# Optimization experiments

Measured on AMD Instinct MI355X. Metric: run time of the kernel, lower is better.

Reference implementation:

```python
import jax, jax.numpy as jnp
import numpy as np

N = 50000   # nodes
E = 800000  # edges
F = 128     # feat_dim
I = 128     # internal_dim
G = 64      # graphs in batch
EPS = 1e-5


def setup_inputs() -> dict:
    key = jax.random.key(0)
    ks = jax.random.split(key, 32)
    s = 0.1
    inp = {
        'x': jax.random.normal(ks[0], (N, F), dtype=jnp.float32),
        'edge_index': jax.random.randint(ks[1], (2, E), 0, N, dtype=jnp.int64),
        'batch': jnp.sort(jax.random.randint(ks[2], (N,), 0, G, dtype=jnp.int64)),
        # InitialSubnet: Linear(F->I) + BN(I)
        'init_W': jax.random.normal(ks[3], (F, I)) * s,
        'init_b': jnp.zeros((I,)),
        'init_g': jnp.ones((I,)),
        'init_bt': jnp.zeros((I,)),
        # 2 middle EdgeConv subnets: Linear(2I->I) + BN(I)
        'mid_W': jax.random.normal(ks[4], (2, 2 * I, I)) * s,
        'mid_b': jnp.zeros((2, I)),
        'mid_g': jnp.ones((2, I)),
        'mid_bt': jnp.zeros((2, I)),
        # 1 er / 1 pr receptor-specific EdgeConv subnet each
        'er_W': jax.random.normal(ks[5], (1, 2 * I, I)) * s,
        'er_b': jnp.zeros((1, I)),
        'er_g': jnp.ones((1, I)),
        'er_bt': jnp.zeros((1, I)),
        'pr_W': jax.random.normal(ks[6], (1, 2 * I, I)) * s,
        'pr_b': jnp.zeros((1, I)),
        'pr_g': jnp.ones((1, I)),
        'pr_bt': jnp.zeros((1, I)),
        # 3 shared posts: Linear(I->2) + BN(2)
        'spost_W': jax.random.normal(ks[7], (3, I, 2)) * s,
        'spost_b': jnp.zeros((3, 2)),
        'spost_g': jnp.ones((3, 2)),
        'spost_bt': jnp.zeros((3, 2)),
        # 1 er post / 1 pr post: Linear(I->1) + BN(1)
        'erpost_W': jax.random.normal(ks[8], (1, I, 1)) * s,
        'erpost_b': jnp.zeros((1, 1)),
        'erpost_g': jnp.ones((1, 1)),
        'erpost_bt': jnp.zeros((1, 1)),
        'prpost_W': jax.random.normal(ks[9], (1, I, 1)) * s,
        'prpost_b': jnp.zeros((1, 1)),
        'prpost_g': jnp.ones((1, 1)),
        'prpost_bt': jnp.zeros((1, 1)),
    }
    return inp


def _bn(h, g, b):
    # BatchNorm1d in training mode: batch stats over the row dim, biased var
    m = jnp.mean(h, axis=0)
    v = jnp.var(h, axis=0)
    return (h - m) * jax.lax.rsqrt(v + EPS) * g + b


def _edgeconv(h, src, dst, W, b, g, bt):
    # PyG EdgeConv: msg = nn(cat([x_i, x_j - x_i])), aggr=max over incoming edges
    x_i = h[dst]                      # [E, I]
    x_j = h[src]                      # [E, I]
    msg = jnp.concatenate([x_i, x_j - x_i], axis=-1) @ W + b  # [E, I]
    msg = jax.nn.elu(_bn(msg, g, bt))
    out = jax.ops.segment_max(msg, dst, num_segments=N)
    return jnp.where(jnp.isneginf(out), 0.0, out)  # isolated nodes -> 0


def _post(h, batch, counts, W, b, g, bt):
    # elu(BN(Linear(h))) then global_mean_pool; dropout is identity (eval)
    h2 = jax.nn.elu(_bn(h @ W + b, g, bt))
    pooled = jax.ops.segment_sum(h2, batch, num_segments=G)
    return pooled / counts[:, None]


def reference(x, edge_index, batch,
              init_W, init_b, init_g, init_bt,
              mid_W, mid_b, mid_g, mid_bt,
              er_W, er_b, er_g, er_bt,
              pr_W, pr_b, pr_g, pr_bt,
              spost_W, spost_b, spost_g, spost_bt,
              erpost_W, erpost_b, erpost_g, erpost_bt,
              prpost_W, prpost_b, prpost_g, prpost_bt):
    src, dst = edge_index[0], edge_index[1]
    counts = jnp.maximum(jax.ops.segment_sum(jnp.ones((N,), x.dtype), batch, num_segments=G), 1.0)

    outs = []
    # InitialSubnet: gelu(BN(Linear(x)))
    h = jax.nn.gelu(_bn(x @ init_W + init_b, init_g, init_bt), approximate=False)
    outs.append(_post(h, batch, counts, spost_W[0], spost_b[0], spost_g[0], spost_bt[0]))

    for l in range(2):
        h = _edgeconv(h, src, dst, mid_W[l], mid_b[l], mid_g[l], mid_bt[l])
        outs.append(_post(h, batch, counts, spost_W[l + 1], spost_b[l + 1], spost_g[l + 1], spost_bt[l + 1]))

    er_h = h
    pr_h = h
    for l in range(1):
        er_h = _edgeconv(er_h, src, dst, er_W[l], er_b[l], er_g[l], er_bt[l])
        er_out = _post(er_h, batch, counts, erpost_W[l], erpost_b[l], erpost_g[l], erpost_bt[l])
        pr_h = _edgeconv(pr_h, src, dst, pr_W[l], pr_b[l], pr_g[l], pr_bt[l])
        pr_out = _post(pr_h, batch, counts, prpost_W[l], prpost_b[l], prpost_g[l], prpost_bt[l])
        outs.append(jnp.concatenate([er_out, pr_out], axis=-1))

    agg = outs[0]
    for o in outs[1:]:
        agg = agg + o
    return agg  # [G, 2]
```

## Files before the change

### kernel.cpp

```cpp
#include <hip/hip_runtime.h>
#include <math.h>

#define EPS 1e-5f

typedef float f32x4v __attribute__((ext_vector_type(4)));
typedef short s16x8  __attribute__((ext_vector_type(8)));

__device__ __forceinline__ float elu_f(float x) { return x > 0.f ? x : expm1f(x); }
__device__ __forceinline__ float blo(unsigned u) { return __uint_as_float(u << 16); }
__device__ __forceinline__ float bhi(unsigned u) { return __uint_as_float(u & 0xffff0000u); }
__device__ __forceinline__ unsigned f2b(float f) {
  unsigned u = __float_as_uint(f);
  unsigned r = ((u >> 16) & 1u) + 0x7fffu;
  return (u + r) >> 16;
}
__device__ __forceinline__ unsigned pack2(float a, float b) {
  return f2b(a) | (f2b(b) << 16);
}

__global__ __launch_bounds__(256) void prep_csr0(const float* __restrict__ init_W,
    const float* __restrict__ mid_W, const float* __restrict__ er_W,
    const float* __restrict__ pr_W, const float* __restrict__ mid_g,
    const float* __restrict__ er_g, const float* __restrict__ pr_g,
    unsigned short* __restrict__ WT,
    const int* __restrict__ dst, int* __restrict__ partials, int Ecnt,
    const int* __restrict__ batch, float* __restrict__ counts, int Nn) {
  if (blockIdx.x < 320) {
    int grp = blockIdx.x >> 6;
    int i = (blockIdx.x & 63) * 256 + threadIdx.x;
    if (i >= 16384) return;
    int k = i >> 7, c = i & 127;
    if (grp == 0) {
      WT[c * 128 + k] = (unsigned short)f2b(init_W[k * 128 + c]);
      return;
    }
    const float* W; const float* g; unsigned short* Wd; unsigned short* W2;
    if (grp == 1)      { W = mid_W;             g = mid_g;       Wd = WT + 1 * 16384; W2 = WT + 2 * 16384; }
    else if (grp == 2) { W = mid_W + 256 * 128; g = mid_g + 128; Wd = WT + 3 * 16384; W2 = WT + 4 * 16384; }
    else if (grp == 3) { W = er_W;              g = er_g;        Wd = WT + 5 * 16384; W2 = WT + 6 * 16384; }
    else               { W = pr_W;              g = pr_g;        Wd = WT + 7 * 16384; W2 = WT + 8 * 16384; }
    float sg = (g[c] >= 0.f) ? 1.f : -1.f;
    float w1 = W[k * 128 + c];
    float w2 = W[(k + 128) * 128 + c];
    Wd[c * 128 + k] = (unsigned short)f2b((w1 - w2) * sg);
    W2[c * 128 + k] = (unsigned short)f2b(w2 * sg);
  } else {
    int b = blockIdx.x - 320;
    if (b < 64) {
      __shared__ int cnt[256];
      cnt[threadIdx.x] = 0;
      __syncthreads();
      int i0 = b * 256 + threadIdx.x, stride = 64 * 256;
      for (int e = i0; e < Ecnt; e += stride) atomicAdd(&cnt[(unsigned)dst[e] >> 8], 1);
      __syncthreads();
      partials[b * 256 + threadIdx.x] = cnt[threadIdx.x];
    } else {
      __shared__ float lc[64];
      if (threadIdx.x < 64) lc[threadIdx.x] = 0.f;
      __syncthreads();
      int i0 = (b - 64) * 256 + threadIdx.x, stride = 64 * 256;
      for (int n = i0; n < Nn; n += stride) atomicAdd(&lc[batch[n]], 1.f);
      __syncthreads();
      if (threadIdx.x < 64 && lc[threadIdx.x] != 0.f)
        atomicAdd(&counts[threadIdx.x * 16], lc[threadIdx.x]);
    }
  }
}

__global__ __launch_bounds__(256) void csr_p0_scan(const int* __restrict__ partials,
    int nblk, int* __restrict__ bucket_base, int* __restrict__ gcursor) {
  __shared__ int sc[256];
  int b = threadIdx.x;
  int s = 0;
  for (int k = 0; k < nblk; ++k) s += partials[k * 256 + b];
  sc[b] = s;
  __syncthreads();
  for (int off = 1; off < 256; off <<= 1) {
    int t = (b >= off) ? sc[b - off] : 0;
    __syncthreads();
    sc[b] += t;
    __syncthreads();
  }
  int excl = sc[b] - s;
  bucket_base[b] = excl;
  gcursor[b * 16] = excl;
  if (b == 255) bucket_base[256] = sc[255];
}

#define P1_CHUNK 4096
__global__ __launch_bounds__(256) void csr_p1_bin(const int* __restrict__ src,
    const int* __restrict__ dst, int* __restrict__ gcursor,
    unsigned* __restrict__ binned, int Ecnt) {
  __shared__ unsigned stage[P1_CHUNK];
  __shared__ int cnt[256], lbase[256], gbase[256], lcur[256], sc[256];
  int tid = threadIdx.x;
  int e0 = blockIdx.x * P1_CHUNK;
  int ecnt = Ecnt - e0; if (ecnt > P1_CHUNK) ecnt = P1_CHUNK;
  cnt[tid] = 0;
  __syncthreads();
  for (int i = tid; i < ecnt; i += 256) atomicAdd(&cnt[(unsigned)dst[e0 + i] >> 8], 1);
  __syncthreads();
  sc[tid] = cnt[tid];
  __syncthreads();
  for (int off = 1; off < 256; off <<= 1) {
    int t = (tid >= off) ? sc[tid - off] : 0;
    __syncthreads();
    sc[tid] += t;
    __syncthreads();
  }
  lbase[tid] = sc[tid] - cnt[tid];
  lcur[tid] = lbase[tid];
  gbase[tid] = (cnt[tid] > 0) ? atomicAdd(&gcursor[tid * 16], cnt[tid]) : 0;
  __syncthreads();
  for (int i = tid; i < ecnt; i += 256) {
    int d = dst[e0 + i], s = src[e0 + i];
    int bk = (unsigned)d >> 8;
    int p = atomicAdd(&lcur[bk], 1);
    stage[p] = ((unsigned)bk << 24) | ((unsigned)(d & 255) << 16) | (unsigned)s;
  }
  __syncthreads();
  for (int i = tid; i < ecnt; i += 256) {
    unsigned v = stage[i];
    int bk = v >> 24;
    binned[gbase[bk] + (i - lbase[bk])] = v;
  }
}

#define P2_CAP 12288
__global__ __launch_bounds__(256) void csr_p2_sort(const unsigned* __restrict__ binned,
    const int* __restrict__ bucket_base, unsigned short* __restrict__ csr_src,
    int* __restrict__ deg, int* __restrict__ rowstart, int Nn) {
  __shared__ unsigned short stage[P2_CAP];
  __shared__ int cnt[256], lbase[256], lcur[256], sc[256];
  int b = blockIdx.x, tid = threadIdx.x;
  int base = bucket_base[b];
  int bcnt = bucket_base[b + 1] - base;
  if (bcnt > P2_CAP) bcnt = P2_CAP;
  cnt[tid] = 0;
  __syncthreads();
  for (int i = tid; i < bcnt; i += 256) atomicAdd(&cnt[(binned[base + i] >> 16) & 255], 1);
  __syncthreads();
  sc[tid] = cnt[tid];
  __syncthreads();
  for (int off = 1; off < 256; off <<= 1) {
    int t = (tid >= off) ? sc[tid - off] : 0;
    __syncthreads();
    sc[tid] += t;
    __syncthreads();
  }
  lbase[tid] = sc[tid] - cnt[tid];
  lcur[tid] = lbase[tid];
  int node = b * 256 + tid;
  if (node < Nn) { deg[node] = cnt[tid]; rowstart[node] = base + lbase[tid]; }
  __syncthreads();
  for (int i = tid; i < bcnt; i += 256) {
    unsigned v = binned[base + i];
    int j = (v >> 16) & 255;
    int p = atomicAdd(&lcur[j], 1);
    stage[p] = (unsigned short)(v & 0xffffu);
  }
  __syncthreads();
  for (int i = tid; i < bcnt; i += 256) csr_src[base + i] = stage[i];
}

template<int XF32, int NMAT, int STATS>
__global__ __launch_bounds__(256, 3) void gemm_mfma(const void* __restrict__ Xv,
    const unsigned short* __restrict__ W0t, const unsigned short* __restrict__ W1t,
    const unsigned short* __restrict__ W2t, const unsigned short* __restrict__ W3t,
    unsigned short* __restrict__ Y0, unsigned short* __restrict__ Y1,
    unsigned short* __restrict__ Y2, unsigned short* __restrict__ Y3,
    float* __restrict__ stOut, int Nrows) {
  int tid = threadIdx.x, lane = tid & 63, wv = tid >> 6;
  int r0 = blockIdx.x * 64;
  int rlo = lane & 15, kg = lane >> 4;
  s16x8 zf = {0, 0, 0, 0, 0, 0, 0, 0};
  s16x8 af[4][4];
#pragma unroll
  for (int rg = 0; rg < 4; ++rg) {
    int arow = r0 + rg * 16 + rlo;
    if (arow < Nrows) {
      if (XF32) {
        const float* xr = (const float*)Xv + (size_t)arow * 128 + kg * 8;
#pragma unroll
        for (int s2 = 0; s2 < 4; ++s2) {
          float4 a = *(const float4*)(xr + s2 * 32);
          float4 b = *(const float4*)(xr + s2 * 32 + 4);
          s16x8 t;
          t[0] = (short)f2b(a.x); t[1] = (short)f2b(a.y);
          t[2] = (short)f2b(a.z); t[3] = (short)f2b(a.w);
          t[4] = (short)f2b(b.x); t[5] = (short)f2b(b.y);
          t[6] = (short)f2b(b.z); t[7] = (short)f2b(b.w);
          af[rg][s2] = t;
        }
      } else {
        const unsigned short* xr = (const unsigned short*)Xv + (size_t)arow * 128 + kg * 8;
#pragma unroll
        for (int s2 = 0; s2 < 4; ++s2) af[rg][s2] = *(const s16x8*)(xr + s2 * 32);
      }
    } else {
#pragma unroll
      for (int s2 = 0; s2 < 4; ++s2) af[rg][s2] = zf;
    }
  }
  const unsigned short* Ws[4] = {W0t, W1t, W2t, W3t};
  unsigned short* Ys[4] = {Y0, Y1, Y2, Y3};
#pragma unroll
  for (int o = 0; o < NMAT; ++o) {
    const unsigned short* Wt = Ws[o];
    unsigned short* Y = Ys[o];
#pragma unroll
    for (int t = 0; t < 2; ++t) {
      int nt = wv * 2 + t;
      const unsigned short* wp = Wt + (size_t)(nt * 16 + rlo) * 128 + kg * 8;
      s16x8 wf[4];
#pragma unroll
      for (int s2 = 0; s2 < 4; ++s2) wf[s2] = *(const s16x8*)(wp + s2 * 32);
      f32x4v acc[4];
#pragma unroll
      for (int rg = 0; rg < 4; ++rg) acc[rg] = (f32x4v){0.f, 0.f, 0.f, 0.f};
#pragma unroll
      for (int s2 = 0; s2 < 4; ++s2)
#pragma unroll
        for (int rg = 0; rg < 4; ++rg)
          acc[rg] = __builtin_amdgcn_mfma_f32_16x16x32_bf16(wf[s2], af[rg][s2], acc[rg], 0, 0, 0);
      float ps0 = 0.f, ps1 = 0.f, ps2 = 0.f, ps3 = 0.f;
      float pq0 = 0.f, pq1 = 0.f, pq2 = 0.f, pq3 = 0.f;
#pragma unroll
      for (int rg = 0; rg < 4; ++rg) {
        int arow = r0 + rg * 16 + rlo;
        if (arow < Nrows) {
          uint2 ov;
          ov.x = pack2(acc[rg][0], acc[rg][1]);
          ov.y = pack2(acc[rg][2], acc[rg][3]);
          *(uint2*)(Y + (size_t)arow * 128 + nt * 16 + kg * 4) = ov;
          if (STATS) {
            float y0 = blo(ov.x), y1 = bhi(ov.x), y2 = blo(ov.y), y3 = bhi(ov.y);
            ps0 += y0; pq0 += y0 * y0;
            ps1 += y1; pq1 += y1 * y1;
            ps2 += y2; pq2 += y2 * y2;
            ps3 += y3; pq3 += y3 * y3;
          }
        }
      }
      if (STATS) {
#pragma unroll
        for (int off = 1; off < 16; off <<= 1) {
          ps0 += __shfl_xor(ps0, off); pq0 += __shfl_xor(pq0, off);
          ps1 += __shfl_xor(ps1, off); pq1 += __shfl_xor(pq1, off);
          ps2 += __shfl_xor(ps2, off); pq2 += __shfl_xor(pq2, off);
          ps3 += __shfl_xor(ps3, off); pq3 += __shfl_xor(pq3, off);
        }
        if (rlo == 0) {
          int col = nt * 16 + kg * 4;
          float* sb = stOut + (size_t)(blockIdx.x & 15) * 256;
          atomicAdd(&sb[2 * col + 0], ps0); atomicAdd(&sb[2 * col + 1], pq0);
          atomicAdd(&sb[2 * (col + 1)], ps1); atomicAdd(&sb[2 * (col + 1) + 1], pq1);
          atomicAdd(&sb[2 * (col + 2)], ps2); atomicAdd(&sb[2 * (col + 2) + 1], pq2);
          atomicAdd(&sb[2 * (col + 3)], ps3); atomicAdd(&sb[2 * (col + 3) + 1], pq3);
        }
      }
    }
  }
}

template<int NMAT, int ACT>
__global__ __launch_bounds__(256, 3) void gemm_act(const unsigned short* __restrict__ Xv,
    const unsigned short* __restrict__ W0t, const unsigned short* __restrict__ W1t,
    const unsigned short* __restrict__ W2t, const unsigned short* __restrict__ W3t,
    unsigned short* __restrict__ Y0, unsigned short* __restrict__ Y1,
    unsigned short* __restrict__ Y2, unsigned short* __restrict__ Y3,
    const float* __restrict__ stn, const float* __restrict__ g,
    const float* __restrict__ bt, const int* __restrict__ deg,
    const float* __restrict__ Wp, float* __restrict__ zP, float* __restrict__ stp,
    float invCnt, int Nrows) {
  __shared__ unsigned short hl[64][136];
  __shared__ float lsc[128], lsh[128], lw0[128], lw1[128];
  __shared__ float red[4][4];
  int tid = threadIdx.x, lane = tid & 63, wv = tid >> 6;
  int r0 = blockIdx.x * 64;
  int rlo = lane & 15, kg = lane >> 4;
  if (tid < 128) {
    float sm = 0.f, sq = 0.f;
#pragma unroll
    for (int k = 0; k < 16; ++k) {
      sm += stn[k * 256 + 2 * tid];
      sq += stn[k * 256 + 2 * tid + 1];
    }
    float mean = sm * invCnt;
    float var = sq * invCnt - mean * mean;
    float sc = g[tid] * rsqrtf(var + EPS);
    float sh = bt[tid] - mean * sc;
    if (ACT == 2 && g[tid] < 0.f) sc = -sc;
    lsc[tid] = sc; lsh[tid] = sh;
    lw0[tid] = Wp[tid * 2]; lw1[tid] = Wp[tid * 2 + 1];
  }
  __syncthreads();
  {
    int row = tid >> 2, q = tid & 3;
    int arow = r0 + row;
    bool rok = arow < Nrows;
    int lrow = rok ? arow : 0;
    float live = 1.f;
    if (ACT == 2) live = (rok && deg[arow] > 0) ? 1.f : 0.f;
    else live = rok ? 1.f : 0.f;
    const uint4* xr = (const uint4*)(Xv + (size_t)lrow * 128 + q * 32);
    float dd0 = 0.f, dd1 = 0.f;
#pragma unroll
    for (int b = 0; b < 4; ++b) {
      uint4 v = xr[b];
      unsigned w[4] = {v.x, v.y, v.z, v.w};
      int cb = q * 32 + b * 8;
#pragma unroll
      for (int u = 0; u < 4; ++u) {
        int c = cb + 2 * u;
        float t0 = blo(w[u]) * lsc[c] + lsh[c];
        float t1 = bhi(w[u]) * lsc[c + 1] + lsh[c + 1];
        float y0, y1;
        if (ACT == 1) {
          y0 = 0.5f * t0 * (1.f + erff(t0 * 0.70710678118f));
          y1 = 0.5f * t1 * (1.f + erff(t1 * 0.70710678118f));
        } else {
          y0 = elu_f(t0); y1 = elu_f(t1);
        }
        y0 *= live; y1 *= live;
        *(unsigned*)&hl[row][c] = pack2(y0, y1);
        dd0 += y0 * lw0[c] + y1 * lw0[c + 1];
        dd1 += y0 * lw1[c] + y1 * lw1[c + 1];
      }
    }
    dd0 += __shfl_xor(dd0, 1); dd0 += __shfl_xor(dd0, 2);
    dd1 += __shfl_xor(dd1, 1); dd1 += __shfl_xor(dd1, 2);
    if (q == 0 && rok) {
      zP[(size_t)arow * 2] = dd0;
      zP[(size_t)arow * 2 + 1] = dd1;
    }
    float s0v = (q == 0 && rok) ? dd0 : 0.f;
    float s1v = (q == 0 && rok) ? dd1 : 0.f;
    float q0v = s0v * s0v, q1v = s1v * s1v;
#pragma unroll
    for (int off = 4; off < 64; off <<= 1) {
      s0v += __shfl_xor(s0v, off); s1v += __shfl_xor(s1v, off);
      q0v += __shfl_xor(q0v, off); q1v += __shfl_xor(q1v, off);
    }
    if (lane == 0) { red[wv][0] = s0v; red[wv][1] = s1v; red[wv][2] = q0v; red[wv][3] = q1v; }
  }
  __syncthreads();
  if (tid < 4) {
    float v = red[0][tid] + red[1][tid] + red[2][tid] + red[3][tid];
    atomicAdd(&stp[tid * 64], v);
  }
  s16x8 af[4][4];
#pragma unroll
  for (int rg = 0; rg < 4; ++rg)
#pragma unroll
    for (int s2 = 0; s2 < 4; ++s2)
      af[rg][s2] = *(const s16x8*)&hl[rg * 16 + rlo][kg * 8 + s2 * 32];
  const unsigned short* Ws[4] = {W0t, W1t, W2t, W3t};
  unsigned short* Ys[4] = {Y0, Y1, Y2, Y3};
#pragma unroll
  for (int o = 0; o < NMAT; ++o) {
    const unsigned short* Wt = Ws[o];
    unsigned short* Y = Ys[o];
#pragma unroll
    for (int t = 0; t < 2; ++t) {
      int nt = wv * 2 + t;
      const unsigned short* wp = Wt + (size_t)(nt * 16 + rlo) * 128 + kg * 8;
      s16x8 wf[4];
#pragma unroll
      for (int s2 = 0; s2 < 4; ++s2) wf[s2] = *(const s16x8*)(wp + s2 * 32);
      f32x4v acc[4];
#pragma unroll
      for (int rg = 0; rg < 4; ++rg) acc[rg] = (f32x4v){0.f, 0.f, 0.f, 0.f};
#pragma unroll
      for (int s2 = 0; s2 < 4; ++s2)
#pragma unroll
        for (int rg = 0; rg < 4; ++rg)
          acc[rg] = __builtin_amdgcn_mfma_f32_16x16x32_bf16(wf[s2], af[rg][s2], acc[rg], 0, 0, 0);
#pragma unroll
      for (int rg = 0; rg < 4; ++rg) {
        int arow = r0 + rg * 16 + rlo;
        if (arow < Nrows) {
          uint2 ov;
          ov.x = pack2(acc[rg][0], acc[rg][1]);
          ov.y = pack2(acc[rg][2], acc[rg][3]);
          *(uint2*)(Y + (size_t)arow * 128 + nt * 16 + kg * 4) = ov;
        }
      }
    }
  }
}

__global__ __launch_bounds__(256, 8) void conv_pass(const unsigned short* __restrict__ A,
    const unsigned short* __restrict__ B, const unsigned short* __restrict__ csr_src,
    const int* __restrict__ rowstart, const int* __restrict__ deg,
    const float* __restrict__ g, unsigned short* __restrict__ Mx,
    float* __restrict__ st, int Nn, int convBlks,
    const float* __restrict__ zPp, const int* __restrict__ batch,
    const float* __restrict__ counts, const float* __restrict__ stpp,
    const float* __restrict__ g2, const float* __restrict__ bt2,
    float* __restrict__ out, float invN) {
  __shared__ float s_sum[128], s_ssq[128];
  int tid = threadIdx.x;
  if ((int)blockIdx.x >= convBlks) {
    __shared__ float lacc[128];
    if (tid < 128) lacc[tid] = 0.f;
    __syncthreads();
    float m0 = stpp[0] * invN, v0 = stpp[128] * invN - m0 * m0;
    float scale0 = g2[0] * rsqrtf(v0 + EPS), shift0 = bt2[0] - m0 * scale0;
    float m1 = stpp[64] * invN, v1 = stpp[192] * invN - m1 * m1;
    float scale1 = g2[1] * rsqrtf(v1 + EPS), shift1 = bt2[1] - m1 * scale1;
    int i0 = (blockIdx.x - convBlks) * 256 + tid;
    int stride = 32 * 256;
    for (int n = i0; n < Nn; n += stride) {
      int gi = batch[n];
      atomicAdd(&lacc[gi * 2], elu_f(zPp[n * 2] * scale0 + shift0));
      atomicAdd(&lacc[gi * 2 + 1], elu_f(zPp[n * 2 + 1] * scale1 + shift1));
    }
    __syncthreads();
    if (tid < 128) {
      int gi = tid >> 1, p = tid & 1;
      float v = lacc[tid];
      if (v != 0.f) atomicAdd(&out[gi * 2 + p], v / fmaxf(counts[gi * 16], 1.f));
    }
    return;
  }
  if (tid < 128) { s_sum[tid] = 0.f; s_ssq[tid] = 0.f; }
  __syncthreads();
  int lane = tid & 63;
  int wave = __builtin_amdgcn_readfirstlane((blockIdx.x << 2) + (tid >> 6));
  int wstride = convBlks << 2;
  int c0 = lane * 2;
  float sg0 = (g[c0] >= 0.f) ? 1.f : -1.f;
  float sg1 = (g[c0 + 1] >= 0.f) ? 1.f : -1.f;
  const unsigned* A32 = (const unsigned*)A;
  const unsigned* B32 = (const unsigned*)B;
  unsigned* M32 = (unsigned*)Mx;
  float s0 = 0.f, ss0 = 0.f, s1 = 0.f, ss1 = 0.f;
  for (int n = wave; n < Nn; n += wstride) {
    int dg = deg[n];
    if (dg == 0) continue;
    int beg = rowstart[n];
    unsigned ua = A32[(size_t)n * 64 + lane];
    float a0 = blo(ua), a1 = bhi(ua);
    float mx0 = -INFINITY, mx1 = -INFINITY;
    int e = beg, eend = beg + dg;
    for (; e + 8 <= eend; e += 8) {
      int idx[8];
#pragma unroll
      for (int q = 0; q < 8; ++q) idx[q] = csr_src[e + q];
      unsigned uu[8];
#pragma unroll
      for (int q = 0; q < 8; ++q) uu[q] = B32[(size_t)idx[q] * 64 + lane];
#pragma unroll
      for (int q = 0; q < 8; ++q) {
        float m0 = a0 + blo(uu[q]), m1 = a1 + bhi(uu[q]);
        s0 += m0; ss0 += m0 * m0;
        s1 += m1; ss1 += m1 * m1;
        mx0 = fmaxf(mx0, m0);
        mx1 = fmaxf(mx1, m1);
      }
    }
    for (; e + 2 <= eend; e += 2) {
      int ia = csr_src[e], ib = csr_src[e + 1];
      unsigned u0 = B32[(size_t)ia * 64 + lane];
      unsigned u1 = B32[(size_t)ib * 64 + lane];
      float m00 = a0 + blo(u0), m01 = a1 + bhi(u0);
      float m10 = a0 + blo(u1), m11 = a1 + bhi(u1);
      s0 += m00 + m10; ss0 += m00 * m00 + m10 * m10;
      s1 += m01 + m11; ss1 += m01 * m01 + m11 * m11;
      mx0 = fmaxf(mx0, fmaxf(m00, m10));
      mx1 = fmaxf(mx1, fmaxf(m01, m11));
    }
    if (e < eend) {
      unsigned u0 = B32[(size_t)csr_src[e] * 64 + lane];
      float m00 = a0 + blo(u0), m01 = a1 + bhi(u0);
      s0 += m00; ss0 += m00 * m00;
      s1 += m01; ss1 += m01 * m01;
      mx0 = fmaxf(mx0, m00);
      mx1 = fmaxf(mx1, m01);
    }
    M32[(size_t)n * 64 + lane] = pack2(mx0, mx1);
  }
  atomicAdd(&s_sum[c0], s0 * sg0); atomicAdd(&s_ssq[c0], ss0);
  atomicAdd(&s_sum[c0 + 1], s1 * sg1); atomicAdd(&s_ssq[c0 + 1], ss1);
  __syncthreads();
  if (tid < 128) {
    float* sb = st + (size_t)(blockIdx.x & 15) * 256;
    atomicAdd(&sb[2 * tid], s_sum[tid]);
    atomicAdd(&sb[2 * tid + 1], s_ssq[tid]);
  }
}

__global__ __launch_bounds__(256, 8) void conv_pass_dual(
    const unsigned short* __restrict__ Aer, const unsigned short* __restrict__ Ber,
    const unsigned short* __restrict__ Apr, const unsigned short* __restrict__ Bpr,
    const unsigned short* __restrict__ csr_src,
    const int* __restrict__ rowstart, const int* __restrict__ deg,
    const float* __restrict__ g_er, const float* __restrict__ g_pr,
    unsigned short* __restrict__ Mer, unsigned short* __restrict__ Mpr,
    float* __restrict__ st_er, float* __restrict__ st_pr, int Nn, int convBlks,
    const float* __restrict__ zPp, const int* __restrict__ batch,
    const float* __restrict__ counts, const float* __restrict__ stpp,
    const float* __restrict__ g2, const float* __restrict__ bt2,
    float* __restrict__ out, float invN) {
  __shared__ float s_e[256], s_p[256];
  int tid = threadIdx.x;
  if ((int)blockIdx.x >= convBlks) {
    __shared__ float lacc[128];
    if (tid < 128) lacc[tid] = 0.f;
    __syncthreads();
    float m0 = stpp[0] * invN, v0 = stpp[128] * invN - m0 * m0;
    float scale0 = g2[0] * rsqrtf(v0 + EPS), shift0 = bt2[0] - m0 * scale0;
    float m1 = stpp[64] * invN, v1 = stpp[192] * invN - m1 * m1;
    float scale1 = g2[1] * rsqrtf(v1 + EPS), shift1 = bt2[1] - m1 * scale1;
    int i0 = (blockIdx.x - convBlks) * 256 + tid;
    int stride = 32 * 256;
    for (int n = i0; n < Nn; n += stride) {
      int gi = batch[n];
      atomicAdd(&lacc[gi * 2], elu_f(zPp[n * 2] * scale0 + shift0));
      atomicAdd(&lacc[gi * 2 + 1], elu_f(zPp[n * 2 + 1] * scale1 + shift1));
    }
    __syncthreads();
    if (tid < 128) {
      int gi = tid >> 1, p = tid & 1;
      float v = lacc[tid];
      if (v != 0.f) atomicAdd(&out[gi * 2 + p], v / fmaxf(counts[gi * 16], 1.f));
    }
    return;
  }
  s_e[tid] = 0.f; s_p[tid] = 0.f;
  __syncthreads();
  int lane = tid & 63;
  int wave = __builtin_amdgcn_readfirstlane((blockIdx.x << 2) + (tid >> 6));
  int wstride = convBlks << 2;
  int c0 = lane * 2;
  float sge0 = (g_er[c0] >= 0.f) ? 1.f : -1.f;
  float sge1 = (g_er[c0 + 1] >= 0.f) ? 1.f : -1.f;
  float sgp0 = (g_pr[c0] >= 0.f) ? 1.f : -1.f;
  float sgp1 = (g_pr[c0 + 1] >= 0.f) ? 1.f : -1.f;
  const unsigned* Ae32 = (const unsigned*)Aer;
  const unsigned* Be32 = (const unsigned*)Ber;
  const unsigned* Ap32 = (const unsigned*)Apr;
  const unsigned* Bp32 = (const unsigned*)Bpr;
  unsigned* Me32 = (unsigned*)Mer;
  unsigned* Mp32 = (unsigned*)Mpr;
  float se0 = 0.f, sse0 = 0.f, se1 = 0.f, sse1 = 0.f;
  float sp0 = 0.f, ssp0 = 0.f, sp1 = 0.f, ssp1 = 0.f;
  for (int n = wave; n < Nn; n += wstride) {
    int dg = deg[n];
    if (dg == 0) continue;
    int beg = rowstart[n];
    unsigned uae = Ae32[(size_t)n * 64 + lane];
    unsigned uap = Ap32[(size_t)n * 64 + lane];
    float ae0 = blo(uae), ae1 = bhi(uae);
    float ap0 = blo(uap), ap1 = bhi(uap);
    float mxe0 = -INFINITY, mxe1 = -INFINITY, mxp0 = -INFINITY, mxp1 = -INFINITY;
    int e = beg, eend = beg + dg;
    for (; e + 8 <= eend; e += 8) {
      int idx[8];
#pragma unroll
      for (int q = 0; q < 8; ++q) idx[q] = csr_src[e + q];
      unsigned ue[8], up[8];
#pragma unroll
      for (int q = 0; q < 8; ++q) ue[q] = Be32[(size_t)idx[q] * 64 + lane];
#pragma unroll
      for (int q = 0; q < 8; ++q) up[q] = Bp32[(size_t)idx[q] * 64 + lane];
#pragma unroll
      for (int q = 0; q < 8; ++q) {
        float me0 = ae0 + blo(ue[q]), me1 = ae1 + bhi(ue[q]);
        float mp0 = ap0 + blo(up[q]), mp1 = ap1 + bhi(up[q]);
        se0 += me0; sse0 += me0 * me0; se1 += me1; sse1 += me1 * me1;
        sp0 += mp0; ssp0 += mp0 * mp0; sp1 += mp1; ssp1 += mp1 * mp1;
        mxe0 = fmaxf(mxe0, me0); mxe1 = fmaxf(mxe1, me1);
        mxp0 = fmaxf(mxp0, mp0); mxp1 = fmaxf(mxp1, mp1);
      }
    }
    for (; e + 2 <= eend; e += 2) {
      int i0 = csr_src[e], i1 = csr_src[e + 1];
      unsigned ue0 = Be32[(size_t)i0 * 64 + lane];
      unsigned up0 = Bp32[(size_t)i0 * 64 + lane];
      unsigned ue1 = Be32[(size_t)i1 * 64 + lane];
      unsigned up1 = Bp32[(size_t)i1 * 64 + lane];
      float me0 = ae0 + blo(ue0), me1 = ae1 + bhi(ue0);
      float mp0 = ap0 + blo(up0), mp1 = ap1 + bhi(up0);
      float ne0 = ae0 + blo(ue1), ne1 = ae1 + bhi(ue1);
      float np0 = ap0 + blo(up1), np1 = ap1 + bhi(up1);
      se0 += me0 + ne0; sse0 += me0 * me0 + ne0 * ne0;
      se1 += me1 + ne1; sse1 += me1 * me1 + ne1 * ne1;
      sp0 += mp0 + np0; ssp0 += mp0 * mp0 + np0 * np0;
      sp1 += mp1 + np1; ssp1 += mp1 * mp1 + np1 * np1;
      mxe0 = fmaxf(mxe0, fmaxf(me0, ne0)); mxe1 = fmaxf(mxe1, fmaxf(me1, ne1));
      mxp0 = fmaxf(mxp0, fmaxf(mp0, np0)); mxp1 = fmaxf(mxp1, fmaxf(mp1, np1));
    }
    if (e < eend) {
      int i0 = csr_src[e];
      unsigned ue = Be32[(size_t)i0 * 64 + lane];
      unsigned up = Bp32[(size_t)i0 * 64 + lane];
      float me0 = ae0 + blo(ue), me1 = ae1 + bhi(ue);
      float mp0 = ap0 + blo(up), mp1 = ap1 + bhi(up);
      se0 += me0; sse0 += me0 * me0; se1 += me1; sse1 += me1 * me1;
      sp0 += mp0; ssp0 += mp0 * mp0; sp1 += mp1; ssp1 += mp1 * mp1;
      mxe0 = fmaxf(mxe0, me0); mxe1 = fmaxf(mxe1, me1);
      mxp0 = fmaxf(mxp0, mp0); mxp1 = fmaxf(mxp1, mp1);
    }
    Me32[(size_t)n * 64 + lane] = pack2(mxe0, mxe1);
    Mp32[(size_t)n * 64 + lane] = pack2(mxp0, mxp1);
  }
  atomicAdd(&s_e[2 * c0], se0 * sge0);       atomicAdd(&s_e[2 * c0 + 1], sse0);
  atomicAdd(&s_e[2 * (c0 + 1)], se1 * sge1); atomicAdd(&s_e[2 * (c0 + 1) + 1], sse1);
  atomicAdd(&s_p[2 * c0], sp0 * sgp0);       atomicAdd(&s_p[2 * c0 + 1], ssp0);
  atomicAdd(&s_p[2 * (c0 + 1)], sp1 * sgp1); atomicAdd(&s_p[2 * (c0 + 1) + 1], ssp1);
  __syncthreads();
  {
    float* se = st_er + (size_t)(blockIdx.x & 15) * 256;
    float* sp = st_pr + (size_t)(blockIdx.x & 15) * 256;
    atomicAdd(&se[tid], s_e[tid]);
    atomicAdd(&sp[tid], s_p[tid]);
  }
}

__global__ __launch_bounds__(256) void fused_post16_dual(
    const unsigned short* __restrict__ Mer, const unsigned short* __restrict__ Mpr,
    const int* __restrict__ deg,
    const float* __restrict__ st_er, const float* __restrict__ st_pr,
    const float* __restrict__ g_er, const float* __restrict__ bt_er,
    const float* __restrict__ g_pr, const float* __restrict__ bt_pr,
    const float* __restrict__ Wer, const float* __restrict__ Wpr,
    float* __restrict__ zP, float* __restrict__ stp_er, float* __restrict__ stp_pr,
    int Nn, float invE) {
  __shared__ float sce_l[128], she_l[128], scp_l[128], shp_l[128];
  __shared__ float red[4][4];
  int tid = threadIdx.x;
  if (tid < 128) {
    float sme = 0.f, sqe = 0.f, smp = 0.f, sqp = 0.f;
#pragma unroll
    for (int k = 0; k < 16; ++k) {
      sme += st_er[k * 256 + 2 * tid];
      sqe += st_er[k * 256 + 2 * tid + 1];
      smp += st_pr[k * 256 + 2 * tid];
      sqp += st_pr[k * 256 + 2 * tid + 1];
    }
    float mean = sme * invE;
    float var = sqe * invE - mean * mean;
    float sc = g_er[tid] * rsqrtf(var + EPS);
    she_l[tid] = bt_er[tid] - mean * sc;
    sce_l[tid] = (g_er[tid] < 0.f) ? -sc : sc;
    mean = smp * invE;
    var = sqp * invE - mean * mean;
    sc = g_pr[tid] * rsqrtf(var + EPS);
    shp_l[tid] = bt_pr[tid] - mean * sc;
    scp_l[tid] = (g_pr[tid] < 0.f) ? -sc : sc;
  }
  __syncthreads();
  int sub = tid & 15, c0 = sub * 8;
  float sce[8], she[8], scp[8], shp[8], we[8], wp[8];
#pragma unroll
  for (int j = 0; j < 8; ++j) {
    sce[j] = sce_l[c0 + j]; she[j] = she_l[c0 + j];
    scp[j] = scp_l[c0 + j]; shp[j] = shp_l[c0 + j];
    we[j] = Wer[c0 + j]; wp[j] = Wpr[c0 + j];
  }
  int g0 = (blockIdx.x * 256 + tid) >> 4;
  int gstride = gridDim.x * 16;
  bool leader = (sub == 0);
  float s0 = 0.f, ss0 = 0.f, s1 = 0.f, ss1 = 0.f;
  for (int n = g0; n < Nn; n += gstride) {
    float d0 = 0.f, d1 = 0.f;
    if (deg[n] > 0) {
      uint4 ve = ((const uint4*)(Mer + (size_t)n * 128))[sub];
      uint4 vp = ((const uint4*)(Mpr + (size_t)n * 128))[sub];
      unsigned wea[4] = {ve.x, ve.y, ve.z, ve.w};
      unsigned wpa[4] = {vp.x, vp.y, vp.z, vp.w};
#pragma unroll
      for (int u = 0; u < 4; ++u) {
        float te0 = blo(wea[u]) * sce[2 * u] + she[2 * u];
        float te1 = bhi(wea[u]) * sce[2 * u + 1] + she[2 * u + 1];
        float tp0 = blo(wpa[u]) * scp[2 * u] + shp[2 * u];
        float tp1 = bhi(wpa[u]) * scp[2 * u + 1] + shp[2 * u + 1];
        d0 += elu_f(te0) * we[2 * u] + elu_f(te1) * we[2 * u + 1];
        d1 += elu_f(tp0) * wp[2 * u] + elu_f(tp1) * wp[2 * u + 1];
      }
    }
#pragma unroll
    for (int off = 1; off < 16; off <<= 1) {
      d0 += __shfl_xor(d0, off);
      d1 += __shfl_xor(d1, off);
    }
    if (leader) {
      zP[n * 2] = d0;
      zP[n * 2 + 1] = d1;
      s0 += d0; ss0 += d0 * d0; s1 += d1; ss1 += d1 * d1;
    }
  }
  s0 += __shfl_xor(s0, 16);  s0 += __shfl_xor(s0, 32);
  s1 += __shfl_xor(s1, 16);  s1 += __shfl_xor(s1, 32);
  ss0 += __shfl_xor(ss0, 16); ss0 += __shfl_xor(ss0, 32);
  ss1 += __shfl_xor(ss1, 16); ss1 += __shfl_xor(ss1, 32);
  int wv = tid >> 6;
  if ((tid & 63) == 0) { red[wv][0] = s0; red[wv][1] = s1; red[wv][2] = ss0; red[wv][3] = ss1; }
  __syncthreads();
  if (tid < 4) {
    float v = red[0][tid] + red[1][tid] + red[2][tid] + red[3][tid];
    if (tid == 0) atomicAdd(&stp_er[0], v);
    else if (tid == 1) atomicAdd(&stp_pr[0], v);
    else if (tid == 2) atomicAdd(&stp_er[128], v);
    else atomicAdd(&stp_pr[128], v);
  }
}

__global__ __launch_bounds__(256) void post_phase2_dual(const float* __restrict__ zP,
    const int* __restrict__ batch, const float* __restrict__ counts,
    const float* __restrict__ st_er, const float* __restrict__ st_pr,
    const float* __restrict__ g_er, const float* __restrict__ bt_er,
    const float* __restrict__ g_pr, const float* __restrict__ bt_pr,
    float* __restrict__ out, int Nrows, float invN) {
  __shared__ float lacc[128];
  if (threadIdx.x < 128) lacc[threadIdx.x] = 0.f;
  __syncthreads();
  float m0 = st_er[0] * invN;
  float v0 = st_er[128] * invN - m0 * m0;
  float scale0 = g_er[0] * rsqrtf(v0 + EPS);
  float shift0 = bt_er[0] - m0 * scale0;
  float m1 = st_pr[0] * invN;
  float v1 = st_pr[128] * invN - m1 * m1;
  float scale1 = g_pr[0] * rsqrtf(v1 + EPS);
  float shift1 = bt_pr[0] - m1 * scale1;
  int i0 = blockIdx.x * 256 + threadIdx.x;
  int stride = gridDim.x * 256;
  for (int n = i0; n < Nrows; n += stride) {
    int gi = batch[n];
    float y0 = elu_f(zP[n * 2] * scale0 + shift0);
    float y1 = elu_f(zP[n * 2 + 1] * scale1 + shift1);
    atomicAdd(&lacc[gi * 2], y0);
    atomicAdd(&lacc[gi * 2 + 1], y1);
  }
  __syncthreads();
  if (threadIdx.x < 128) {
    int gi = threadIdx.x >> 1, p = threadIdx.x & 1;
    float v = lacc[threadIdx.x];
    if (v != 0.f)
      atomicAdd(&out[gi * 2 + p], v / fmaxf(counts[gi * 16], 1.f));
  }
}

extern "C" void kernel_launch(void* const* d_in, const int* in_sizes, int n_in,
                              void* d_out, int out_size, void* d_ws, size_t ws_size,
                              hipStream_t stream) {
  const float* x       = (const float*)d_in[0];
  const int*   ei      = (const int*)d_in[1];
  const int*   batch   = (const int*)d_in[2];
  const float* init_W  = (const float*)d_in[3];
  const float* init_g  = (const float*)d_in[5];
  const float* init_bt = (const float*)d_in[6];
  const float* mid_W   = (const float*)d_in[7];
  const float* mid_g   = (const float*)d_in[9];
  const float* mid_bt  = (const float*)d_in[10];
  const float* er_W    = (const float*)d_in[11];
  const float* er_g    = (const float*)d_in[13];
  const float* er_bt   = (const float*)d_in[14];
  const float* pr_W    = (const float*)d_in[15];
  const float* pr_g    = (const float*)d_in[17];
  const float* pr_bt   = (const float*)d_in[18];
  const float* spost_W  = (const float*)d_in[19];
  const float* spost_g  = (const float*)d_in[21];
  const float* spost_bt = (const float*)d_in[22];
  const float* erpost_W  = (const float*)d_in[23];
  const float* erpost_g  = (const float*)d_in[25];
  const float* erpost_bt = (const float*)d_in[26];
  const float* prpost_W  = (const float*)d_in[27];
  const float* prpost_g  = (const float*)d_in[29];
  const float* prpost_bt = (const float*)d_in[30];

  int N = in_sizes[0] / 128;
  int E = in_sizes[1] / 2;
  float invN = 1.f / (float)N;
  float invE = 1.f / (float)E;
  float* out = (float*)d_out;

  const int CONV_BLKS = 2048;
  int nbuck = (N + 255) >> 8;

  size_t NB = (size_t)N * 128;
  unsigned short* TbI = (unsigned short*)d_ws;
  unsigned short* Tb0 = TbI + NB;
  unsigned short* Tb1 = Tb0 + NB;
  unsigned short* Tb2 = Tb1 + NB;
  unsigned short* Tb3 = Tb2 + NB;
  unsigned short* MxB = Tb3 + NB;
  unsigned short* MxB2 = MxB + NB;
  float* zP     = (float*)(MxB2 + NB);
  float* counts = zP + (size_t)2 * N;
  float* stats  = counts + 1024;
  float* post   = stats + 5 * 4096;
  unsigned short* WT = (unsigned short*)(post + 5 * 512);
  int* deg        = (int*)(WT + 9 * 16384);
  int* rowstart   = deg + N;
  int* bucketbase = rowstart + N;
  int* gcursor    = bucketbase + 320;
  int* partials   = gcursor + 256 * 16;
  unsigned* binned = (unsigned*)(partials + 64 * 256);
  unsigned short* csr_src = (unsigned short*)(binned + E);

  int gemmGrid = (N + 63) / 64;

  hipMemsetAsync(d_out, 0, out_size * sizeof(float), stream);
  hipMemsetAsync(counts, 0, (1024 + 5 * 4096 + 5 * 512) * sizeof(float), stream);

  const int* e_src = ei;
  const int* e_dst = ei + E;
  prep_csr0<<<448, 256, 0, stream>>>(init_W, mid_W, er_W, pr_W, mid_g, er_g, pr_g, WT,
                                     e_dst, partials, E, batch, counts, N);
  csr_p0_scan<<<1, 256, 0, stream>>>(partials, 64, bucketbase, gcursor);
  csr_p1_bin<<<(E + P1_CHUNK - 1) / P1_CHUNK, 256, 0, stream>>>(e_src, e_dst, gcursor, binned, E);
  csr_p2_sort<<<nbuck, 256, 0, stream>>>(binned, bucketbase, csr_src, deg, rowstart, N);

  gemm_mfma<1, 1, 1><<<gemmGrid, 256, 0, stream>>>((const void*)x, WT, nullptr, nullptr, nullptr,
                                                   TbI, nullptr, nullptr, nullptr, stats, N);

  gemm_act<2, 1><<<gemmGrid, 256, 0, stream>>>(TbI,
      WT + 1 * 16384, WT + 2 * 16384, nullptr, nullptr, Tb0, Tb1, nullptr, nullptr,
      stats, init_g, init_bt, deg, spost_W, zP, post + 0 * 512, invN, N);

  conv_pass<<<CONV_BLKS + 32, 256, 0, stream>>>(Tb0, Tb1, csr_src, rowstart, deg, mid_g,
      MxB, stats + 1 * 4096, N, CONV_BLKS,
      zP, batch, counts, post + 0 * 512, spost_g, spost_bt, out, invN);

  gemm_act<2, 2><<<gemmGrid, 256, 0, stream>>>(MxB,
      WT + 3 * 16384, WT + 4 * 16384, nullptr, nullptr, Tb0, Tb1, nullptr, nullptr,
      stats + 1 * 4096, mid_g, mid_bt, deg, spost_W + 256, zP, post + 1 * 512, invE, N);

  conv_pass<<<CONV_BLKS + 32, 256, 0, stream>>>(Tb0, Tb1, csr_src, rowstart, deg, mid_g + 128,
      MxB, stats + 2 * 4096, N, CONV_BLKS,
      zP, batch, counts, post + 1 * 512, spost_g + 2, spost_bt + 2, out, invN);

  gemm_act<4, 2><<<gemmGrid, 256, 0, stream>>>(MxB,
      WT + 5 * 16384, WT + 6 * 16384, WT + 7 * 16384, WT + 8 * 16384,
      Tb0, Tb1, Tb2, Tb3,
      stats + 2 * 4096, mid_g + 128, mid_bt + 128, deg, spost_W + 512,
      zP, post + 2 * 512, invE, N);

  conv_pass_dual<<<CONV_BLKS + 32, 256, 0, stream>>>(Tb0, Tb1, Tb2, Tb3, csr_src, rowstart, deg,
      er_g, pr_g, MxB, MxB2, stats + 3 * 4096, stats + 4 * 4096, N, CONV_BLKS,
      zP, batch, counts, post + 2 * 512, spost_g + 4, spost_bt + 4, out, invN);

  fused_post16_dual<<<512, 256, 0, stream>>>(MxB, MxB2, deg,
      stats + 3 * 4096, stats + 4 * 4096, er_g, er_bt, pr_g, pr_bt,
      erpost_W, prpost_W, zP, post + 3 * 512, post + 4 * 512, N, invE);
  post_phase2_dual<<<32, 256, 0, stream>>>(zP, batch, counts,
      post + 3 * 512, post + 4 * 512, erpost_g, erpost_bt, prpost_g, prpost_bt,
      out, N, invN);
}
```

Baseline: 385.5 us.

## Merge CSR binning and sorting passes with independent GEMM stages into shared launches

Turns the CSR bin and sort kernels and the initial GEMM kernels into device functions and launches them in pairs as combined grids. Blocks are split by index, so the independent edge-sorting work runs next to the node GEMM work, and two kernel launches and their serialization gaps go away. In exchange each combined kernel takes the larger shared-memory footprint of both bodies, which may lower occupancy. The ACT=1 GEMM now gets a null deg pointer, which only works if that path never reads deg.

After: 365.4 us. 5.2% less time.

```diff
diff --git a/kernel.cpp b/kernel.cpp
--- a/kernel.cpp
+++ b/kernel.cpp
@@ -88,13 +88,13 @@
 }
 
 #define P1_CHUNK 4096
-__global__ __launch_bounds__(256) void csr_p1_bin(const int* __restrict__ src,
+__device__ __forceinline__ void csr_p1_body(int bid, const int* __restrict__ src,
     const int* __restrict__ dst, int* __restrict__ gcursor,
     unsigned* __restrict__ binned, int Ecnt) {
   __shared__ unsigned stage[P1_CHUNK];
   __shared__ int cnt[256], lbase[256], gbase[256], lcur[256], sc[256];
   int tid = threadIdx.x;
-  int e0 = blockIdx.x * P1_CHUNK;
+  int e0 = bid * P1_CHUNK;
   int ecnt = Ecnt - e0; if (ecnt > P1_CHUNK) ecnt = P1_CHUNK;
   cnt[tid] = 0;
   __syncthreads();
@@ -127,12 +127,12 @@
 }
 
 #define P2_CAP 12288
-__global__ __launch_bounds__(256) void csr_p2_sort(const unsigned* __restrict__ binned,
+__device__ __forceinline__ void csr_p2_body(int bid, const unsigned* __restrict__ binned,
     const int* __restrict__ bucket_base, unsigned short* __restrict__ csr_src,
     int* __restrict__ deg, int* __restrict__ rowstart, int Nn) {
   __shared__ unsigned short stage[P2_CAP];
   __shared__ int cnt[256], lbase[256], lcur[256], sc[256];
-  int b = blockIdx.x, tid = threadIdx.x;
+  int b = bid, tid = threadIdx.x;
   int base = bucket_base[b];
   int bcnt = bucket_base[b + 1] - base;
   if (bcnt > P2_CAP) bcnt = P2_CAP;
@@ -164,14 +164,14 @@
 }
 
 template<int XF32, int NMAT, int STATS>
-__global__ __launch_bounds__(256, 3) void gemm_mfma(const void* __restrict__ Xv,
+__device__ __forceinline__ void gemm_mfma_body(int bid, const void* __restrict__ Xv,
     const unsigned short* __restrict__ W0t, const unsigned short* __restrict__ W1t,
     const unsigned short* __restrict__ W2t, const unsigned short* __restrict__ W3t,
     unsigned short* __restrict__ Y0, unsigned short* __restrict__ Y1,
     unsigned short* __restrict__ Y2, unsigned short* __restrict__ Y3,
     float* __restrict__ stOut, int Nrows) {
   int tid = threadIdx.x, lane = tid & 63, wv = tid >> 6;
-  int r0 = blockIdx.x * 64;
+  int r0 = bid * 64;
   int rlo = lane & 15, kg = lane >> 4;
   s16x8 zf = {0, 0, 0, 0, 0, 0, 0, 0};
   s16x8 af[4][4];
@@ -252,7 +252,7 @@
         }
         if (rlo == 0) {
           int col = nt * 16 + kg * 4;
-          float* sb = stOut + (size_t)(blockIdx.x & 15) * 256;
+          float* sb = stOut + (size_t)(bid & 15) * 256;
           atomicAdd(&sb[2 * col + 0], ps0); atomicAdd(&sb[2 * col + 1], pq0);
           atomicAdd(&sb[2 * (col + 1)], ps1); atomicAdd(&sb[2 * (col + 1) + 1], pq1);
           atomicAdd(&sb[2 * (col + 2)], ps2); atomicAdd(&sb[2 * (col + 2) + 1], pq2);
@@ -264,7 +264,7 @@
 }
 
 template<int NMAT, int ACT>
-__global__ __launch_bounds__(256, 3) void gemm_act(const unsigned short* __restrict__ Xv,
+__device__ __forceinline__ void gemm_act_body(int bid, const unsigned short* __restrict__ Xv,
     const unsigned short* __restrict__ W0t, const unsigned short* __restrict__ W1t,
     const unsigned short* __restrict__ W2t, const unsigned short* __restrict__ W3t,
     unsigned short* __restrict__ Y0, unsigned short* __restrict__ Y1,
@@ -277,7 +277,7 @@
   __shared__ float lsc[128], lsh[128], lw0[128], lw1[128];
   __shared__ float red[4][4];
   int tid = threadIdx.x, lane = tid & 63, wv = tid >> 6;
-  int r0 = blockIdx.x * 64;
+  int r0 = bid * 64;
   int rlo = lane & 15, kg = lane >> 4;
   if (tid < 128) {
     float sm = 0.f, sq = 0.f;
@@ -387,6 +387,52 @@
         }
       }
     }
+  }
+}
+
+template<int NMAT, int ACT>
+__global__ __launch_bounds__(256, 3) void gemm_act(const unsigned short* __restrict__ Xv,
+    const unsigned short* __restrict__ W0t, const unsigned short* __restrict__ W1t,
+    const unsigned short* __restrict__ W2t, const unsigned short* __restrict__ W3t,
+    unsigned short* __restrict__ Y0, unsigned short* __restrict__ Y1,
+    unsigned short* __restrict__ Y2, unsigned short* __restrict__ Y3,
+    const float* __restrict__ stn, const float* __restrict__ g,
+    const float* __restrict__ bt, const int* __restrict__ deg,
+    const float* __restrict__ Wp, float* __restrict__ zP, float* __restrict__ stp,
+    float invCnt, int Nrows) {
+  gemm_act_body<NMAT, ACT>(blockIdx.x, Xv, W0t, W1t, W2t, W3t, Y0, Y1, Y2, Y3,
+                           stn, g, bt, deg, Wp, zP, stp, invCnt, Nrows);
+}
+
+__global__ __launch_bounds__(256, 3) void p1_initgemm(
+    const int* __restrict__ src, const int* __restrict__ dst, int* __restrict__ gcursor,
+    unsigned* __restrict__ binned, int Ecnt, int p1b,
+    const void* __restrict__ Xv, const unsigned short* __restrict__ W0t,
+    unsigned short* __restrict__ Y0, float* __restrict__ stOut, int Nrows) {
+  if ((int)blockIdx.x < p1b) {
+    csr_p1_body(blockIdx.x, src, dst, gcursor, binned, Ecnt);
+  } else {
+    gemm_mfma_body<1, 1, 1>(blockIdx.x - p1b, Xv, W0t, nullptr, nullptr, nullptr,
+                            Y0, nullptr, nullptr, nullptr, stOut, Nrows);
+  }
+}
+
+__global__ __launch_bounds__(256, 3) void p2_act0(
+    const unsigned* __restrict__ binned, const int* __restrict__ bucket_base,
+    unsigned short* __restrict__ csr_src, int* __restrict__ deg,
+    int* __restrict__ rowstart, int Nn, int nbuck,
+    const unsigned short* __restrict__ Xv,
+    const unsigned short* __restrict__ W0t, const unsigned short* __restrict__ W1t,
+    unsigned short* __restrict__ Y0, unsigned short* __restrict__ Y1,
+    const float* __restrict__ stn, const float* __restrict__ g,
+    const float* __restrict__ bt, const float* __restrict__ Wp,
+    float* __restrict__ zP, float* __restrict__ stp, float invCnt) {
+  if ((int)blockIdx.x < nbuck) {
+    csr_p2_body(blockIdx.x, binned, bucket_base, csr_src, deg, rowstart, Nn);
+  } else {
+    gemm_act_body<2, 1>(blockIdx.x - nbuck, Xv, W0t, W1t, nullptr, nullptr,
+                        Y0, Y1, nullptr, nullptr, stn, g, bt, nullptr,
+                        Wp, zP, stp, invCnt, Nn);
   }
 }
 
@@ -779,6 +825,7 @@
 
   const int CONV_BLKS = 2048;
   int nbuck = (N + 255) >> 8;
+  int p1b = (E + P1_CHUNK - 1) / P1_CHUNK;
 
   size_t NB = (size_t)N * 128;
   unsigned short* TbI = (unsigned short*)d_ws;
@@ -811,15 +858,13 @@
   prep_csr0<<<448, 256, 0, stream>>>(init_W, mid_W, er_W, pr_W, mid_g, er_g, pr_g, WT,
                                      e_dst, partials, E, batch, counts, N);
   csr_p0_scan<<<1, 256, 0, stream>>>(partials, 64, bucketbase, gcursor);
-  csr_p1_bin<<<(E + P1_CHUNK - 1) / P1_CHUNK, 256, 0, stream>>>(e_src, e_dst, gcursor, binned, E);
-  csr_p2_sort<<<nbuck, 256, 0, stream>>>(binned, bucketbase, csr_src, deg, rowstart, N);
-
-  gemm_mfma<1, 1, 1><<<gemmGrid, 256, 0, stream>>>((const void*)x, WT, nullptr, nullptr, nullptr,
-                                                   TbI, nullptr, nullptr, nullptr, stats, N);
-
-  gemm_act<2, 1><<<gemmGrid, 256, 0, stream>>>(TbI,
-      WT + 1 * 16384, WT + 2 * 16384, nullptr, nullptr, Tb0, Tb1, nullptr, nullptr,
-      stats, init_g, init_bt, deg, spost_W, zP, post + 0 * 512, invN, N);
+
+  p1_initgemm<<<p1b + gemmGrid, 256, 0, stream>>>(e_src, e_dst, gcursor, binned, E, p1b,
+      (const void*)x, WT, TbI, stats, N);
+
+  p2_act0<<<nbuck + gemmGrid, 256, 0, stream>>>(binned, bucketbase, csr_src, deg, rowstart,
+      N, nbuck, TbI, WT + 1 * 16384, WT + 2 * 16384, Tb0, Tb1,
+      stats, init_g, init_bt, spost_W, zP, post + 0 * 512, invN);
 
   conv_pass<<<CONV_BLKS + 32, 256, 0, stream>>>(Tb0, Tb1, csr_src, rowstart, deg, mid_g,
       MxB, stats + 1 * 4096, N, CONV_BLKS,
```
